# Performance work log

Hardware: AMD Instinct MI355X
Metric: run time of the kernel (lower is better)

## Reference

```python
import jax, jax.numpy as jnp
import numpy as np
from jax import lax

SIGMA = 4.0
RADIUS = int(4.0 * SIGMA + 0.5)  # scipy gaussian_filter default truncate=4.0 -> radius 16


def _gaussian_kernel1d(sigma, radius):
    x = jnp.arange(-radius, radius + 1, dtype=jnp.float32)
    phi = jnp.exp(-0.5 * (x / sigma) ** 2)
    return phi / phi.sum()


def _gaussian_blur(img):
    # img: [B, H, W]; scipy mode='reflect' == numpy pad mode='symmetric'
    k = _gaussian_kernel1d(SIGMA, RADIUS)
    K = 2 * RADIUS + 1
    x = jnp.pad(img, ((0, 0), (RADIUS, RADIUS), (RADIUS, RADIUS)), mode='symmetric')[:, None]  # [B,1,H+2r,W+2r]
    x = lax.conv_general_dilated(x, k.reshape(1, 1, K, 1), (1, 1), 'VALID')  # blur rows
    x = lax.conv_general_dilated(x, k.reshape(1, 1, 1, K), (1, 1), 'VALID')  # blur cols
    return x[:, 0]


def setup_inputs() -> dict:
    key = jax.random.key(0)
    k1, k2, k3 = jax.random.split(key, 3)
    B, C, P, h, w, crop = 16, 256, 3136, 56, 56, 224
    embeddings = jax.random.normal(k1, (B, C, P), dtype=jnp.float32)
    means = jax.random.normal(k2, (P, C), dtype=jnp.float32) * 0.1
    # SPD inverse covariance: I + low-rank, so the quadratic form is positive (sqrt-safe)
    u = jax.random.normal(k3, (P, C, 4), dtype=jnp.float32) * 0.1
    inv_cov = jnp.einsum('pcr,pdr->pcd', u, u) + jnp.eye(C, dtype=jnp.float32)
    return {"embeddings": embeddings, "means": means, "inv_cov": inv_cov,
            "h": h, "w": w, "crop_size": crop}


def reference(embeddings, means, inv_cov, h, w, crop_size):
    # embeddings: [B, C, P], means: [P, C], inv_cov: [P, C, C]
    b = embeddings.shape[0]
    delta = jnp.transpose(embeddings, (0, 2, 1)) - means[None]           # [B, P, C]
    d2 = jnp.einsum('bpc,pcd,bpd->bp', delta, inv_cov, delta)            # Mahalanobis^2
    dist = jnp.sqrt(d2).reshape(b, h, w)
    # F.interpolate(mode='bilinear', align_corners=False) == jax.image.resize bilinear (upsampling)
    score = jax.image.resize(dist, (b, crop_size, crop_size), method='bilinear')
    score = _gaussian_blur(score)
    mn, mx = score.min(), score.max()
    return (score - mn) / (mx - mn)
```

## Files before the change

### kernel.cpp

```cpp
#include <hip/hip_runtime.h>
#include <math.h>

#define NP 3136
#define NC 256
#define NB 16
#define HH 56
#define OW 224

__device__ __forceinline__ void rowstep(const float4 mv, const int c,
                                        const float (&dreg)[4][16], float (&z)[16],
                                        const float (*dc_lds)[20]) {
  float s[16];
#pragma unroll
  for (int b = 0; b < 16; ++b) s[b] = mv.x * dreg[0][b];
#pragma unroll
  for (int b = 0; b < 16; ++b) s[b] = fmaf(mv.y, dreg[1][b], s[b]);
#pragma unroll
  for (int b = 0; b < 16; ++b) s[b] = fmaf(mv.z, dreg[2][b], s[b]);
#pragma unroll
  for (int b = 0; b < 16; ++b) s[b] = fmaf(mv.w, dreg[3][b], s[b]);
#pragma unroll
  for (int q = 0; q < 4; ++q) {
    const float4 dc = *reinterpret_cast<const float4*>(&dc_lds[c][4 * q]);
    z[4 * q + 0] = fmaf(dc.x, s[4 * q + 0], z[4 * q + 0]);
    z[4 * q + 1] = fmaf(dc.y, s[4 * q + 1], z[4 * q + 1]);
    z[4 * q + 2] = fmaf(dc.z, s[4 * q + 2], z[4 * q + 2]);
    z[4 * q + 3] = fmaf(dc.w, s[4 * q + 3], z[4 * q + 3]);
  }
}

__global__ __launch_bounds__(256) void k_dist(const float* __restrict__ emb,
                                              const float* __restrict__ means,
                                              const float* __restrict__ icov,
                                              float* __restrict__ dist,
                                              unsigned int* __restrict__ mm) {
  __shared__ float dc_lds[NC][20];
  __shared__ float db_lds[NB][NC + 8];
  __shared__ float zbuf[4][16];

  const int bid = blockIdx.x;
  const int p = (bid & 7) * (NP >> 3) + (bid >> 3);
  const int t = threadIdx.x;
  const int lane = t & 63;
  const int wv = t >> 6;

  if (bid == 0 && t == 0) { mm[0] = 0x7f800000u; mm[1] = 0u; }

  {
    const int c = t;
    const float mn = means[(size_t)p * NC + c];
    const float* ep = emb + (size_t)c * NP + p;
    float d[16];
#pragma unroll
    for (int b = 0; b < 16; ++b) d[b] = ep[(size_t)b * (NC * NP)] - mn;
#pragma unroll
    for (int q = 0; q < 4; ++q) {
      *reinterpret_cast<float4*>(&dc_lds[c][4 * q]) =
          make_float4(d[4 * q], d[4 * q + 1], d[4 * q + 2], d[4 * q + 3]);
    }
#pragma unroll
    for (int b = 0; b < 16; ++b) db_lds[b][c] = d[b];
  }
  __syncthreads();

  float dreg[4][16];
#pragma unroll
  for (int b = 0; b < 16; ++b) {
    const float4 v = *reinterpret_cast<const float4*>(&db_lds[b][4 * lane]);
    dreg[0][b] = v.x; dreg[1][b] = v.y; dreg[2][b] = v.z; dreg[3][b] = v.w;
  }

  float z[16];
#pragma unroll
  for (int b = 0; b < 16; ++b) z[b] = 0.f;

  const float* mbase = icov + (size_t)p * (NC * NC) + (size_t)(wv * 64) * NC + 4 * lane;
#define LOADM(r) (*reinterpret_cast<const float4*>(mbase + (size_t)(r) * NC))

  float4 m0 = LOADM(0), m1 = LOADM(1), m2 = LOADM(2), m3 = LOADM(3);
  for (int rb = 0; rb < 64; rb += 4) {
    const int r4 = (rb + 4 < 64) ? rb + 4 : 63;
    const int r5 = (rb + 5 < 64) ? rb + 5 : 63;
    const int r6 = (rb + 6 < 64) ? rb + 6 : 63;
    const int r7 = (rb + 7 < 64) ? rb + 7 : 63;
    const float4 n0 = LOADM(r4);
    const float4 n1 = LOADM(r5);
    const float4 n2 = LOADM(r6);
    const float4 n3 = LOADM(r7);
    rowstep(m0, wv * 64 + rb + 0, dreg, z, dc_lds);
    rowstep(m1, wv * 64 + rb + 1, dreg, z, dc_lds);
    rowstep(m2, wv * 64 + rb + 2, dreg, z, dc_lds);
    rowstep(m3, wv * 64 + rb + 3, dreg, z, dc_lds);
    m0 = n0; m1 = n1; m2 = n2; m3 = n3;
  }
#undef LOADM

#pragma unroll
  for (int b = 0; b < 16; ++b) {
    float v = z[b];
#pragma unroll
    for (int off = 32; off > 0; off >>= 1) v += __shfl_xor(v, off, 64);
    z[b] = v;
  }
  if (lane == 0) {
#pragma unroll
    for (int b = 0; b < 16; ++b) zbuf[wv][b] = z[b];
  }
  __syncthreads();
  if (t < 16) {
    const float d2 = zbuf[0][t] + zbuf[1][t] + zbuf[2][t] + zbuf[3][t];
    dist[(size_t)t * NP + p] = sqrtf(d2);
  }
}

__global__ __launch_bounds__(256) void k_blur(const float* __restrict__ dist,
                                              float* __restrict__ outb,
                                              unsigned int* __restrict__ mm) {
  __shared__ float w[33];
  __shared__ float ld[56 * 56];
  __shared__ float ccx[56][13];
  __shared__ float ccy[224][13];
  __shared__ int xlo[56];
  __shared__ int ylo[224];
  __shared__ float rb[56][57];
  __shared__ float red[4][2];

  const int t = threadIdx.x;
  const int b = blockIdx.x >> 2;
  const int x0 = (blockIdx.x & 3) * 56;

  if (t < 33) {
    const float d = (float)(t - 16);
    w[t] = expf(-d * d * (1.f / 32.f));
  }
  for (int i = t; i < 56 * 56; i += 256) ld[i] = dist[(size_t)b * NP + i];
  __syncthreads();

  if (t < 224) {
    const int y = t;
    int lo = 56;
    for (int j = 0; j < 33; ++j) {
      int yy = y + j - 16;
      yy = (yy < 0) ? (-1 - yy) : (yy >= 224 ? 447 - yy : yy);
      const int U = (int)floorf(yy * 0.25f - 0.375f);
      const int u0c = U < 0 ? 0 : U;
      lo = lo < u0c ? lo : u0c;
    }
    ylo[y] = lo;
#pragma unroll
    for (int n = 0; n < 13; ++n) ccy[y][n] = 0.f;
    for (int j = 0; j < 33; ++j) {
      int yy = y + j - 16;
      yy = (yy < 0) ? (-1 - yy) : (yy >= 224 ? 447 - yy : yy);
      const float sy = yy * 0.25f - 0.375f;
      const int U = (int)floorf(sy);
      const float fy = sy - (float)U;
      const int u0c = U < 0 ? 0 : U;
      const int u1c = (U + 1) > 55 ? 55 : (U + 1);
      ccy[y][u0c - lo] += w[j] * (1.f - fy);
      ccy[y][u1c - lo] += w[j] * fy;
    }
  }
  if (t < 56) {
    const int x = x0 + t;
    int lo = 56;
    for (int j = 0; j < 33; ++j) {
      int xx = x + j - 16;
      xx = (xx < 0) ? (-1 - xx) : (xx >= 224 ? 447 - xx : xx);
      const int U = (int)floorf(xx * 0.25f - 0.375f);
      const int u0c = U < 0 ? 0 : U;
      lo = lo < u0c ? lo : u0c;
    }
    xlo[t] = lo;
#pragma unroll
    for (int n = 0; n < 13; ++n) ccx[t][n] = 0.f;
    for (int j = 0; j < 33; ++j) {
      int xx = x + j - 16;
      xx = (xx < 0) ? (-1 - xx) : (xx >= 224 ? 447 - xx : xx);
      const float sx = xx * 0.25f - 0.375f;
      const int U = (int)floorf(sx);
      const float fx = sx - (float)U;
      const int u0c = U < 0 ? 0 : U;
      const int u1c = (U + 1) > 55 ? 55 : (U + 1);
      ccx[t][u0c - lo] += w[j] * (1.f - fx);
      ccx[t][u1c - lo] += w[j] * fx;
    }
  }
  __syncthreads();

  for (int i = t; i < 56 * 56; i += 256) {
    const int u = i / 56, lx = i - 56 * u;
    const int lo = xlo[lx];
    const float* lrow = &ld[u * 56];
    float acc = 0.f;
#pragma unroll
    for (int n = 0; n < 13; ++n) {
      int v = lo + n;
      v = v > 55 ? 55 : v;
      acc = fmaf(ccx[lx][n], lrow[v], acc);
    }
    rb[u][lx] = acc;
  }
  __syncthreads();

  float mnv = 1e30f, mxv = 0.f;
  if (t < 224) {
    const int y = t;
    const int lo = ylo[y];
    float* orow = outb + ((size_t)b * OW + y) * OW + x0;
    for (int c = 0; c < 7; ++c) {
      float a0 = 0.f, a1 = 0.f, a2 = 0.f, a3 = 0.f,
            a4 = 0.f, a5 = 0.f, a6 = 0.f, a7 = 0.f;
#pragma unroll
      for (int n = 0; n < 13; ++n) {
        int u = lo + n;
        u = u > 55 ? 55 : u;
        const float cy = ccy[y][n];
        const float* rrow = &rb[u][c * 8];
        a0 = fmaf(cy, rrow[0], a0); a1 = fmaf(cy, rrow[1], a1);
        a2 = fmaf(cy, rrow[2], a2); a3 = fmaf(cy, rrow[3], a3);
        a4 = fmaf(cy, rrow[4], a4); a5 = fmaf(cy, rrow[5], a5);
        a6 = fmaf(cy, rrow[6], a6); a7 = fmaf(cy, rrow[7], a7);
      }
      orow[c * 8 + 0] = a0; orow[c * 8 + 1] = a1;
      orow[c * 8 + 2] = a2; orow[c * 8 + 3] = a3;
      orow[c * 8 + 4] = a4; orow[c * 8 + 5] = a5;
      orow[c * 8 + 6] = a6; orow[c * 8 + 7] = a7;
      mnv = fminf(mnv, fminf(fminf(fminf(a0, a1), fminf(a2, a3)),
                             fminf(fminf(a4, a5), fminf(a6, a7))));
      mxv = fmaxf(mxv, fmaxf(fmaxf(fmaxf(a0, a1), fmaxf(a2, a3)),
                             fmaxf(fmaxf(a4, a5), fmaxf(a6, a7))));
    }
  }
#pragma unroll
  for (int off = 32; off > 0; off >>= 1) {
    mnv = fminf(mnv, __shfl_xor(mnv, off, 64));
    mxv = fmaxf(mxv, __shfl_xor(mxv, off, 64));
  }
  const int lane = t & 63, wv = t >> 6;
  if (lane == 0) { red[wv][0] = mnv; red[wv][1] = mxv; }
  __syncthreads();
  if (t == 0) {
    const float m0 = fminf(fminf(red[0][0], red[1][0]), fminf(red[2][0], red[3][0]));
    const float m1 = fmaxf(fmaxf(red[0][1], red[1][1]), fmaxf(red[2][1], red[3][1]));
    atomicMin(&mm[0], __float_as_uint(m0));
    atomicMax(&mm[1], __float_as_uint(m1));
  }
}

__global__ __launch_bounds__(256) void k_norm(const float4* __restrict__ in,
                                              const unsigned int* __restrict__ mm,
                                              float4* __restrict__ out) {
  const int i = blockIdx.x * 256 + threadIdx.x;
  const float mn = __uint_as_float(mm[0]);
  const float mx = __uint_as_float(mm[1]);
  const float inv = 1.f / (mx - mn);
  const float4 v = in[i];
  out[i] = make_float4((v.x - mn) * inv, (v.y - mn) * inv,
                       (v.z - mn) * inv, (v.w - mn) * inv);
}

extern "C" void kernel_launch(void* const* d_in, const int* in_sizes, int n_in,
                              void* d_out, int out_size, void* d_ws, size_t ws_size,
                              hipStream_t stream) {
  const float* emb = (const float*)d_in[0];
  const float* means = (const float*)d_in[1];
  const float* icov = (const float*)d_in[2];
  float* out = (float*)d_out;

  char* ws = (char*)d_ws;
  float* dist = (float*)ws;
  float* tmp1 = (float*)(ws + 204800);
  unsigned int* mm = (unsigned int*)(ws + 3416064);

  k_dist<<<NP, 256, 0, stream>>>(emb, means, icov, dist, mm);
  k_blur<<<NB * 4, 256, 0, stream>>>(dist, tmp1, mm);
  k_norm<<<NB * OW * OW / 1024, 256, 0, stream>>>((const float4*)tmp1, mm,
                                                  (float4*)out);
}
```

Measured before the change: 206.0 us.

## Fuse min-max normalization into blur kernel with grid-wide spin barrier

Drops the separate normalization kernel. The blur kernel now keeps its output tile in shared memory, publishes its block's min and max atomically, then spins on a global counter until all 64 blocks have arrived before normalizing and writing the final output with float4 stores. This removes a kernel launch and one full write-then-read pass over the intermediate image. The cost is an inter-block spin barrier, which depends on all 64 blocks being resident at the same time, plus extra shared memory for the tile.

```diff
diff --git a/kernel.cpp b/kernel.cpp
--- a/kernel.cpp
+++ b/kernel.cpp
@@ -44,7 +44,11 @@
   const int lane = t & 63;
   const int wv = t >> 6;
 
-  if (bid == 0 && t == 0) { mm[0] = 0x7f800000u; mm[1] = 0u; }
+  if (bid == 0 && t == 0) {
+    mm[0] = 0x7f800000u;
+    mm[1] = 0u;
+    mm[2] = 0u;
+  }
 
   {
     const int c = t;
@@ -114,7 +118,7 @@
 }
 
 __global__ __launch_bounds__(256) void k_blur(const float* __restrict__ dist,
-                                              float* __restrict__ outb,
+                                              float* __restrict__ out,
                                               unsigned int* __restrict__ mm) {
   __shared__ float w[33];
   __shared__ float ld[56 * 56];
@@ -123,6 +127,7 @@
   __shared__ int xlo[56];
   __shared__ int ylo[224];
   __shared__ float rb[56][57];
+  __shared__ float sout[224][56];
   __shared__ float red[4][2];
 
   const int t = threadIdx.x;
@@ -207,7 +212,6 @@
   if (t < 224) {
     const int y = t;
     const int lo = ylo[y];
-    float* orow = outb + ((size_t)b * OW + y) * OW + x0;
     for (int c = 0; c < 7; ++c) {
       float a0 = 0.f, a1 = 0.f, a2 = 0.f, a3 = 0.f,
             a4 = 0.f, a5 = 0.f, a6 = 0.f, a7 = 0.f;
@@ -222,10 +226,9 @@
         a4 = fmaf(cy, rrow[4], a4); a5 = fmaf(cy, rrow[5], a5);
         a6 = fmaf(cy, rrow[6], a6); a7 = fmaf(cy, rrow[7], a7);
       }
-      orow[c * 8 + 0] = a0; orow[c * 8 + 1] = a1;
-      orow[c * 8 + 2] = a2; orow[c * 8 + 3] = a3;
-      orow[c * 8 + 4] = a4; orow[c * 8 + 5] = a5;
-      orow[c * 8 + 6] = a6; orow[c * 8 + 7] = a7;
+      float* srow = &sout[y][c * 8];
+      srow[0] = a0; srow[1] = a1; srow[2] = a2; srow[3] = a3;
+      srow[4] = a4; srow[5] = a5; srow[6] = a6; srow[7] = a7;
       mnv = fminf(mnv, fminf(fminf(fminf(a0, a1), fminf(a2, a3)),
                              fminf(fminf(a4, a5), fminf(a6, a7))));
       mxv = fmaxf(mxv, fmaxf(fmaxf(fmaxf(a0, a1), fmaxf(a2, a3)),
@@ -240,24 +243,31 @@
   const int lane = t & 63, wv = t >> 6;
   if (lane == 0) { red[wv][0] = mnv; red[wv][1] = mxv; }
   __syncthreads();
+
   if (t == 0) {
     const float m0 = fminf(fminf(red[0][0], red[1][0]), fminf(red[2][0], red[3][0]));
     const float m1 = fmaxf(fmaxf(red[0][1], red[1][1]), fmaxf(red[2][1], red[3][1]));
     atomicMin(&mm[0], __float_as_uint(m0));
     atomicMax(&mm[1], __float_as_uint(m1));
-  }
-}
-
-__global__ __launch_bounds__(256) void k_norm(const float4* __restrict__ in,
-                                              const unsigned int* __restrict__ mm,
-                                              float4* __restrict__ out) {
-  const int i = blockIdx.x * 256 + threadIdx.x;
-  const float mn = __uint_as_float(mm[0]);
-  const float mx = __uint_as_float(mm[1]);
-  const float inv = 1.f / (mx - mn);
-  const float4 v = in[i];
-  out[i] = make_float4((v.x - mn) * inv, (v.y - mn) * inv,
-                       (v.z - mn) * inv, (v.w - mn) * inv);
+    __threadfence();
+    atomicAdd(&mm[2], 1u);
+    while (atomicAdd(&mm[2], 0u) < 64u) {
+    }
+    __threadfence();
+    red[0][0] = __uint_as_float(atomicAdd(&mm[0], 0u));
+    red[0][1] = __uint_as_float(atomicAdd(&mm[1], 0u));
+  }
+  __syncthreads();
+
+  const float gmn = red[0][0];
+  const float inv = 1.f / (red[0][1] - gmn);
+  for (int i = t; i < 224 * 14; i += 256) {
+    const int y = i / 14, c = i - 14 * y;
+    const float* s = &sout[y][c * 4];
+    float4 v = make_float4((s[0] - gmn) * inv, (s[1] - gmn) * inv,
+                           (s[2] - gmn) * inv, (s[3] - gmn) * inv);
+    *reinterpret_cast<float4*>(out + ((size_t)b * OW + y) * OW + x0 + c * 4) = v;
+  }
 }
 
 extern "C" void kernel_launch(void* const* d_in, const int* in_sizes, int n_in,
@@ -270,11 +280,8 @@
 
   char* ws = (char*)d_ws;
   float* dist = (float*)ws;
-  float* tmp1 = (float*)(ws + 204800);
   unsigned int* mm = (unsigned int*)(ws + 3416064);
 
   k_dist<<<NP, 256, 0, stream>>>(emb, means, icov, dist, mm);
-  k_blur<<<NB * 4, 256, 0, stream>>>(dist, tmp1, mm);
-  k_norm<<<NB * OW * OW / 1024, 256, 0, stream>>>((const float4*)tmp1, mm,
-                                                  (float4*)out);
-}
+  k_blur<<<NB * 4, 256, 0, stream>>>(dist, out, mm);
+}
```

Result: no change. 207.1 us (+0.5%).
